# Kernel tuning notes

Hardware: AMD Instinct MI355X
Metric: run time of the kernel (lower is better)

## Reference

```python
import jax, jax.numpy as jnp
import numpy as np

BS, NUM_RELS, NUM_NODES, EMB = 8, 16, 512, 256


def setup_inputs() -> dict:
    key = jax.random.key(0)
    k1, k2, k3, k4 = jax.random.split(key, 4)
    features = jax.random.normal(k1, (BS, NUM_NODES, EMB), dtype=jnp.float32)
    adjacency = jax.random.uniform(k2, (BS, NUM_RELS, NUM_NODES, NUM_NODES), dtype=jnp.float32)
    # xavier_uniform bounds
    bound = float(np.sqrt(6.0 / (EMB + EMB)))
    W_r = jax.random.uniform(k3, (NUM_RELS, EMB, EMB), minval=-bound, maxval=bound, dtype=jnp.float32)
    W_0 = jax.random.uniform(k4, (EMB, EMB), minval=-bound, maxval=bound, dtype=jnp.float32)
    return {"features": features, "adjacency": adjacency, "W_r": W_r, "W_0": W_0}


def reference(features, adjacency, W_r, W_0):
    # msg[b,r,n,d] = sum_m adjacency[b,r,n,m] * features[b,m,d]
    msg = jnp.einsum('brnm,bmd->brnd', adjacency, features)
    # per-relation projection then sum over relations: [b,n,h]
    features_1 = jnp.einsum('brnd,rdh->bnh', msg, W_r)
    features_2 = jnp.einsum('bnd,dh->bnh', features, W_0)
    return jax.nn.relu(features_1 + features_2)
```

## Files before the change

### kernel.cpp

```cpp
#include <hip/hip_runtime.h>
#include <hip/hip_bf16.h>

#define BS   8
#define NREL 16
#define NN   512
#define EMB  256

typedef float f32x4 __attribute__((ext_vector_type(4)));
typedef short s16x8 __attribute__((ext_vector_type(8)));

__device__ __forceinline__ unsigned short f2bf_bits(float f) {
    union { float f; unsigned u; } v; v.f = f;
    unsigned r = (v.u + 0x7FFFu + ((v.u >> 16) & 1u)) >> 16;
    return (unsigned short)r;
}

__global__ __launch_bounds__(256) void k0_transpose(
        const float* __restrict__ Wr, const float* __restrict__ W0,
        unsigned short* __restrict__ wT) {
    __shared__ float tile[32][33];
    int bid = blockIdx.x;
    int rel = bid / 64;
    int t   = bid % 64;
    int d0  = (t & 7) * 32;
    int h0  = (t >> 3) * 32;
    int tx  = threadIdx.x & 31;
    int ty  = threadIdx.x >> 5;
    const float* src = (rel < NREL) ? (Wr + rel * (EMB * EMB)) : W0;
#pragma unroll
    for (int k = 0; k < 4; ++k) {
        int d = d0 + ty + k * 8;
        tile[ty + k * 8][tx] = src[d * EMB + h0 + tx];
    }
    __syncthreads();
#pragma unroll
    for (int k = 0; k < 4; ++k) {
        int h = h0 + ty + k * 8;
        wT[(rel * EMB + h) * EMB + d0 + tx] = f2bf_bits(tile[tx][ty + k * 8]);
    }
}

__global__ __launch_bounds__(256) void k0b_convF(
        const float* __restrict__ F, unsigned short* __restrict__ Fbf) {
    long i = ((long)blockIdx.x * 256 + threadIdx.x) * 8;
    f32x4 x0 = *(const f32x4*)(F + i);
    f32x4 x1 = *(const f32x4*)(F + i + 4);
    s16x8 v;
    v[0] = (short)f2bf_bits(x0[0]); v[1] = (short)f2bf_bits(x0[1]);
    v[2] = (short)f2bf_bits(x0[2]); v[3] = (short)f2bf_bits(x0[3]);
    v[4] = (short)f2bf_bits(x1[0]); v[5] = (short)f2bf_bits(x1[1]);
    v[6] = (short)f2bf_bits(x1[2]); v[7] = (short)f2bf_bits(x1[3]);
    *(s16x8*)(Fbf + i) = v;
}

__global__ __launch_bounds__(256) void k1_fw(
        const unsigned short* __restrict__ Fbf, const unsigned short* __restrict__ wT,
        unsigned short* __restrict__ FW, float* __restrict__ F2f) {
    int bid = blockIdx.x;
    int b   = bid & 7;
    int q   = bid >> 3;
    int rel = q % 17;
    int mt  = q / 17;
    int tid = threadIdx.x;
    int w   = tid >> 6;
    int l   = tid & 63;
    int lg  = l >> 4;
    int lr  = l & 15;

    int h0 = w * 64;
    int m0 = mt * 64;

    const unsigned short* wt = wT + rel * (EMB * EMB);
    const unsigned short* Fb = Fbf + (long)b * (NN * EMB);

    f32x4 acc[4][4];
#pragma unroll
    for (int i = 0; i < 4; ++i)
#pragma unroll
        for (int j = 0; j < 4; ++j) acc[i][j] = (f32x4){0.f, 0.f, 0.f, 0.f};

#pragma unroll 2
    for (int kk = 0; kk < EMB; kk += 32) {
        s16x8 afrag[4];
#pragma unroll
        for (int hi = 0; hi < 4; ++hi) {
            int row = h0 + hi * 16 + lr;
            afrag[hi] = *(const s16x8*)(wt + row * EMB + kk + lg * 8);
        }
        s16x8 bfrag[4];
#pragma unroll
        for (int bi = 0; bi < 4; ++bi) {
            int m = m0 + bi * 16 + lr;
            bfrag[bi] = *(const s16x8*)(Fb + m * EMB + kk + lg * 8);
        }
#pragma unroll
        for (int hi = 0; hi < 4; ++hi)
#pragma unroll
            for (int bi = 0; bi < 4; ++bi)
                acc[hi][bi] = __builtin_amdgcn_mfma_f32_16x16x32_bf16(
                    afrag[hi], bfrag[bi], acc[hi][bi], 0, 0, 0);
    }

#pragma unroll
    for (int hi = 0; hi < 4; ++hi) {
#pragma unroll
        for (int bi = 0; bi < 4; ++bi) {
            int m  = m0 + bi * 16 + lr;
            int kg = m >> 3, ko = m & 7;
#pragma unroll
            for (int j = 0; j < 4; ++j) {
                int h = h0 + hi * 16 + lg * 4 + j;
                if (rel < NREL)
                    FW[(long)((b * 16 + rel) * 64 + kg) * 2048 + h * 8 + ko] =
                        f2bf_bits(acc[hi][bi][j]);
                else
                    F2f[((long)b * NN + m) * EMB + h] = acc[hi][bi][j];
            }
        }
    }
}

__global__ __launch_bounds__(512, 4) void k2_main(
        const float* __restrict__ adj, const unsigned short* __restrict__ FW,
        float* __restrict__ part) {
    __shared__ unsigned short Blds[2][8192];
    int bid = blockIdx.x;
    int b   = bid & 7;
    int t   = bid >> 3;
    int nt  = t & 7;
    int rg  = t >> 3;
    int tid = threadIdx.x;
    int w   = tid >> 6;
    int l   = tid & 63;
    int lg  = l >> 4, lr = l & 15;
    int wr  = w >> 1;
    int wc  = w & 1;

    int nrow = nt * 64 + wr * 16;
    int h0   = wc * 128;

    f32x4 acc[8];
#pragma unroll
    for (int i = 0; i < 8; ++i) acc[i] = (f32x4){0.f, 0.f, 0.f, 0.f};

    const float* adj_base =
        adj + (((long)(b * 16 + rg * 2)) * NN + nrow + lr) * NN + lg * 8;
    const unsigned short* fw_t = FW + (long)(b * 16 + rg * 2) * 131072 + tid * 8;

    f32x4 ax[4], ay[4];
    s16x8 fw0[2], fw1[2];

    fw0[0] = *(const s16x8*)(fw_t);
    fw1[0] = *(const s16x8*)(fw_t + 4096);
    ax[0]  = *(const f32x4*)(adj_base);
    ay[0]  = *(const f32x4*)(adj_base + 4);
    fw0[1] = *(const s16x8*)(fw_t + 8192);
    fw1[1] = *(const s16x8*)(fw_t + 8192 + 4096);
    ax[1]  = *(const f32x4*)(adj_base + 32);
    ay[1]  = *(const f32x4*)(adj_base + 36);
    *(s16x8*)(&Blds[0][tid * 8])        = fw0[0];
    *(s16x8*)(&Blds[0][tid * 8 + 4096]) = fw1[0];
    asm volatile("s_waitcnt lgkmcnt(0)" ::: "memory");
    __builtin_amdgcn_sched_barrier(0);
    __builtin_amdgcn_s_barrier();
    asm volatile("" ::: "memory");

#pragma unroll
    for (int s = 0; s < 32; ++s) {
        if (s + 2 < 32) {
            int sn = s + 2;
            const unsigned short* fsrc =
                fw_t + (long)(sn >> 4) * 131072 + (sn & 15) * 8192;
            fw0[sn & 1] = *(const s16x8*)(fsrc);
            fw1[sn & 1] = *(const s16x8*)(fsrc + 4096);
            const float* pn =
                adj_base + (long)(sn >> 4) * (NN * NN) + (sn & 15) * 32;
            ax[sn & 3] = *(const f32x4*)pn;
            ay[sn & 3] = *(const f32x4*)(pn + 4);
        }

        f32x4 x0 = ax[s & 3], x1 = ay[s & 3];
        s16x8 a;
        a[0] = (short)f2bf_bits(x0[0]); a[1] = (short)f2bf_bits(x0[1]);
        a[2] = (short)f2bf_bits(x0[2]); a[3] = (short)f2bf_bits(x0[3]);
        a[4] = (short)f2bf_bits(x1[0]); a[5] = (short)f2bf_bits(x1[1]);
        a[6] = (short)f2bf_bits(x1[2]); a[7] = (short)f2bf_bits(x1[3]);
        const unsigned short* bl = &Blds[s & 1][lg * 2048];
#pragma unroll
        for (int f = 0; f < 8; ++f) {
            s16x8 bf = *(const s16x8*)(bl + (h0 + f * 16 + lr) * 8);
            acc[f] = __builtin_amdgcn_mfma_f32_16x16x32_bf16(a, bf, acc[f], 0, 0, 0);
        }
        asm volatile("" ::: "memory");

        if (s + 1 < 32) {
            *(s16x8*)(&Blds[(s + 1) & 1][tid * 8])        = fw0[(s + 1) & 1];
            *(s16x8*)(&Blds[(s + 1) & 1][tid * 8 + 4096]) = fw1[(s + 1) & 1];
            asm volatile("s_waitcnt lgkmcnt(0)" ::: "memory");
            __builtin_amdgcn_sched_barrier(0);
            __builtin_amdgcn_s_barrier();
            asm volatile("" ::: "memory");
        }
    }

    float* pp = part + ((long)rg * BS + b) * (NN * EMB);
#pragma unroll
    for (int f = 0; f < 8; ++f) {
        int h = h0 + f * 16 + lr;
#pragma unroll
        for (int j = 0; j < 4; ++j) {
            int n = nrow + lg * 4 + j;
            pp[(long)n * EMB + h] = acc[f][j];
        }
    }
}

__global__ __launch_bounds__(256) void k3_reduce(
        const float* __restrict__ part, const float* __restrict__ F2f,
        float* __restrict__ out) {
    const long PS = (long)BS * NN * EMB;
    long i = ((long)blockIdx.x * 256 + threadIdx.x) * 4;
    f32x4 s = *(const f32x4*)(part + i);
#pragma unroll
    for (int rg = 1; rg < 8; ++rg)
        s += *(const f32x4*)(part + i + (long)rg * PS);
    s += *(const f32x4*)(F2f + i);
    f32x4 r;
#pragma unroll
    for (int j = 0; j < 4; ++j) r[j] = s[j] > 0.f ? s[j] : 0.f;
    *(f32x4*)(out + i) = r;
}

extern "C" void kernel_launch(void* const* d_in, const int* in_sizes, int n_in,
                              void* d_out, int out_size, void* d_ws, size_t ws_size,
                              hipStream_t stream) {
    const float* F   = (const float*)d_in[0];
    const float* adj = (const float*)d_in[1];
    const float* Wr  = (const float*)d_in[2];
    const float* W0  = (const float*)d_in[3];
    float* out = (float*)d_out;

    unsigned short* wT  = (unsigned short*)d_ws;
    unsigned short* Fbf = wT + 17 * 256 * 256;
    unsigned short* FW  = Fbf + (long)8 * 512 * 256;
    float* F2f  = (float*)(FW + (long)8 * 16 * 64 * 2048);
    float* part = F2f + (long)8 * 512 * 256;

    k0_transpose<<<17 * 64, 256, 0, stream>>>(Wr, W0, wT);
    k0b_convF<<<512, 256, 0, stream>>>(F, Fbf);
    k1_fw<<<1088, 256, 0, stream>>>(Fbf, wT, FW, F2f);
    k2_main<<<512, 512, 0, stream>>>(adj, FW, part);
    k3_reduce<<<1024, 256, 0, stream>>>(part, F2f, out);
}
```

Measured before the change: 113.8 us.

## Split K across wave pairs in k2_main and reduce partials through LDS

Each wave now computes all 256 output columns for its 16 rows but handles only alternate K-slices (even or odd by wc), instead of splitting the columns between wave pairs. Each wave therefore converts half as many adjacency elements to bf16, and the adjacency load and conversion per wave drops. Two K-slices are staged per LDS buffer with wider per-thread copies. At the end the two halves are summed through LDS before storing. In exchange accumulator registers double to 16 f32x4, which may hurt occupancy under launch_bounds(512,4), and an extra LDS reduction with two block barriers is added.

```diff
diff --git a/kernel.cpp b/kernel.cpp
--- a/kernel.cpp
+++ b/kernel.cpp
@@ -123,7 +123,7 @@
 __global__ __launch_bounds__(512, 4) void k2_main(
         const float* __restrict__ adj, const unsigned short* __restrict__ FW,
         float* __restrict__ part) {
-    __shared__ unsigned short Blds[2][8192];
+    __shared__ unsigned short Blds[2][2][8192];
     int bid = blockIdx.x;
     int b   = bid & 7;
     int t   = bid >> 3;
@@ -137,65 +137,94 @@
     int wc  = w & 1;
 
     int nrow = nt * 64 + wr * 16;
-    int h0   = wc * 128;
-
-    f32x4 acc[8];
-#pragma unroll
-    for (int i = 0; i < 8; ++i) acc[i] = (f32x4){0.f, 0.f, 0.f, 0.f};
+
+    f32x4 acc[16];
+#pragma unroll
+    for (int i = 0; i < 16; ++i) acc[i] = (f32x4){0.f, 0.f, 0.f, 0.f};
 
     const float* adj_base =
         adj + (((long)(b * 16 + rg * 2)) * NN + nrow + lr) * NN + lg * 8;
-    const unsigned short* fw_t = FW + (long)(b * 16 + rg * 2) * 131072 + tid * 8;
-
-    f32x4 ax[4], ay[4];
-    s16x8 fw0[2], fw1[2];
-
-    fw0[0] = *(const s16x8*)(fw_t);
-    fw1[0] = *(const s16x8*)(fw_t + 4096);
-    ax[0]  = *(const f32x4*)(adj_base);
-    ay[0]  = *(const f32x4*)(adj_base + 4);
-    fw0[1] = *(const s16x8*)(fw_t + 8192);
-    fw1[1] = *(const s16x8*)(fw_t + 8192 + 4096);
-    ax[1]  = *(const f32x4*)(adj_base + 32);
-    ay[1]  = *(const f32x4*)(adj_base + 36);
-    *(s16x8*)(&Blds[0][tid * 8])        = fw0[0];
-    *(s16x8*)(&Blds[0][tid * 8 + 4096]) = fw1[0];
+    int sp = tid >> 8;
+    const unsigned short* fw_s =
+        FW + (long)(b * 16 + rg * 2) * 131072 + (tid & 255) * 32;
+    unsigned short* ldst0 = &Blds[0][sp][(tid & 255) * 32];
+    unsigned short* ldst1 = &Blds[1][sp][(tid & 255) * 32];
+
+    s16x8 fwr0, fwr1, fwr2, fwr3;
+    f32x4 ax0, ay0, ax1, ay1;
+
+    {
+        long off = (long)(sp >> 4) * 131072 + (sp & 15) * 8192;
+        const unsigned short* src = fw_s + off;
+        fwr0 = *(const s16x8*)(src);
+        fwr1 = *(const s16x8*)(src + 8);
+        fwr2 = *(const s16x8*)(src + 16);
+        fwr3 = *(const s16x8*)(src + 24);
+        *(s16x8*)(ldst0)      = fwr0;
+        *(s16x8*)(ldst0 + 8)  = fwr1;
+        *(s16x8*)(ldst0 + 16) = fwr2;
+        *(s16x8*)(ldst0 + 24) = fwr3;
+    }
+    {
+        int sl = wc;
+        const float* p = adj_base + (long)(sl >> 4) * (NN * NN) + (sl & 15) * 32;
+        ax0 = *(const f32x4*)p;
+        ay0 = *(const f32x4*)(p + 4);
+    }
+    {
+        int sl = 2 + sp;
+        long off = (long)(sl >> 4) * 131072 + (sl & 15) * 8192;
+        const unsigned short* src = fw_s + off;
+        fwr0 = *(const s16x8*)(src);
+        fwr1 = *(const s16x8*)(src + 8);
+        fwr2 = *(const s16x8*)(src + 16);
+        fwr3 = *(const s16x8*)(src + 24);
+    }
     asm volatile("s_waitcnt lgkmcnt(0)" ::: "memory");
     __builtin_amdgcn_sched_barrier(0);
     __builtin_amdgcn_s_barrier();
     asm volatile("" ::: "memory");
 
 #pragma unroll
-    for (int s = 0; s < 32; ++s) {
-        if (s + 2 < 32) {
-            int sn = s + 2;
-            const unsigned short* fsrc =
-                fw_t + (long)(sn >> 4) * 131072 + (sn & 15) * 8192;
-            fw0[sn & 1] = *(const s16x8*)(fsrc);
-            fw1[sn & 1] = *(const s16x8*)(fsrc + 4096);
-            const float* pn =
-                adj_base + (long)(sn >> 4) * (NN * NN) + (sn & 15) * 32;
-            ax[sn & 3] = *(const f32x4*)pn;
-            ay[sn & 3] = *(const f32x4*)(pn + 4);
-        }
-
-        f32x4 x0 = ax[s & 3], x1 = ay[s & 3];
+    for (int i = 0; i < 16; ++i) {
+        if (i + 1 < 16) {
+            int sl = 2 * (i + 1) + wc;
+            const float* p =
+                adj_base + (long)(sl >> 4) * (NN * NN) + (sl & 15) * 32;
+            if ((i & 1) == 0) { ax1 = *(const f32x4*)p; ay1 = *(const f32x4*)(p + 4); }
+            else              { ax0 = *(const f32x4*)p; ay0 = *(const f32x4*)(p + 4); }
+        }
+
+        f32x4 x0 = ((i & 1) == 0) ? ax0 : ax1;
+        f32x4 x1 = ((i & 1) == 0) ? ay0 : ay1;
         s16x8 a;
         a[0] = (short)f2bf_bits(x0[0]); a[1] = (short)f2bf_bits(x0[1]);
         a[2] = (short)f2bf_bits(x0[2]); a[3] = (short)f2bf_bits(x0[3]);
         a[4] = (short)f2bf_bits(x1[0]); a[5] = (short)f2bf_bits(x1[1]);
         a[6] = (short)f2bf_bits(x1[2]); a[7] = (short)f2bf_bits(x1[3]);
-        const unsigned short* bl = &Blds[s & 1][lg * 2048];
-#pragma unroll
-        for (int f = 0; f < 8; ++f) {
-            s16x8 bf = *(const s16x8*)(bl + (h0 + f * 16 + lr) * 8);
+        const unsigned short* bl = &Blds[i & 1][wc][lg * 2048];
+#pragma unroll
+        for (int f = 0; f < 16; ++f) {
+            s16x8 bf = *(const s16x8*)(bl + (f * 16 + lr) * 8);
             acc[f] = __builtin_amdgcn_mfma_f32_16x16x32_bf16(a, bf, acc[f], 0, 0, 0);
         }
         asm volatile("" ::: "memory");
 
-        if (s + 1 < 32) {
-            *(s16x8*)(&Blds[(s + 1) & 1][tid * 8])        = fw0[(s + 1) & 1];
-            *(s16x8*)(&Blds[(s + 1) & 1][tid * 8 + 4096]) = fw1[(s + 1) & 1];
+        if (i + 1 < 16) {
+            unsigned short* dst = ((i + 1) & 1) ? ldst1 : ldst0;
+            *(s16x8*)(dst)      = fwr0;
+            *(s16x8*)(dst + 8)  = fwr1;
+            *(s16x8*)(dst + 16) = fwr2;
+            *(s16x8*)(dst + 24) = fwr3;
+            if (i + 2 < 16) {
+                int sl = 2 * (i + 2) + sp;
+                long off = (long)(sl >> 4) * 131072 + (sl & 15) * 8192;
+                const unsigned short* src = fw_s + off;
+                fwr0 = *(const s16x8*)(src);
+                fwr1 = *(const s16x8*)(src + 8);
+                fwr2 = *(const s16x8*)(src + 16);
+                fwr3 = *(const s16x8*)(src + 24);
+            }
             asm volatile("s_waitcnt lgkmcnt(0)" ::: "memory");
             __builtin_amdgcn_sched_barrier(0);
             __builtin_amdgcn_s_barrier();
@@ -203,14 +232,27 @@
         }
     }
 
-    float* pp = part + ((long)rg * BS + b) * (NN * EMB);
-#pragma unroll
-    for (int f = 0; f < 8; ++f) {
-        int h = h0 + f * 16 + lr;
-#pragma unroll
-        for (int j = 0; j < 4; ++j) {
-            int n = nrow + lg * 4 + j;
-            pp[(long)n * EMB + h] = acc[f][j];
+    __syncthreads();
+    float* lf = (float*)Blds;
+    if (wc == 1) {
+#pragma unroll
+        for (int f = 0; f < 16; ++f)
+#pragma unroll
+            for (int j = 0; j < 4; ++j)
+                lf[wr * 4096 + (f * 4 + j) * 64 + l] = acc[f][j];
+    }
+    __syncthreads();
+    if (wc == 0) {
+        float* pp = part + ((long)rg * BS + b) * (NN * EMB);
+#pragma unroll
+        for (int f = 0; f < 16; ++f) {
+            int h = f * 16 + lr;
+#pragma unroll
+            for (int j = 0; j < 4; ++j) {
+                int n = nrow + lg * 4 + j;
+                float v = acc[f][j] + lf[wr * 4096 + (f * 4 + j) * 64 + l];
+                pp[(long)n * EMB + h] = v;
+            }
         }
     }
 }
```

Result: slower. 118.5 us (+4.1%).
